# Kernel optimization log

Hardware: AMD Instinct MI355X
Metric: run time of the kernel (lower is better)

## Reference

```python
import jax, jax.numpy as jnp
import numpy as np
from jax import lax
from jax.scipy.special import logsumexp

N = 1024   # keypoints image 0
M = 1024   # keypoints image 1
D = 256    # descriptor dim
H = 4      # attention heads
L = 18     # GNN layers ('self','cross')*9
ITERS = 100
KENC = [4, 32, 64, 128, 256]


def conv1(x, w, b):
    # 1x1 Conv1d == channel matmul: x [b,c,n], w [o,c], b [o]
    return jnp.einsum('oc,bcn->bon', w, x) + b[None, :, None]


def inorm(x, eps=1e-5):
    # InstanceNorm1d (affine=False): normalize over length per (b, c)
    m = jnp.mean(x, axis=-1, keepdims=True)
    v = jnp.var(x, axis=-1, keepdims=True)
    return (x - m) * lax.rsqrt(v + eps)


def attention_block(x, src, pw, pb, mw, mb):
    b, d, _ = x.shape
    dh = d // H
    q = conv1(x, pw[0], pb[0]).reshape(b, dh, H, -1)
    k = conv1(src, pw[1], pb[1]).reshape(b, dh, H, -1)
    v = conv1(src, pw[2], pb[2]).reshape(b, dh, H, -1)
    s = jnp.einsum('bdhn,bdhm->bhnm', q, k) / (dh ** 0.5)
    p = jax.nn.softmax(s, axis=-1)
    o = jnp.einsum('bhnm,bdhm->bdhn', p, v).reshape(b, d, -1)
    return conv1(o, mw, mb)


def prop(x, src, i, Pw, Pb, Mw, Mb, W0, B0, W1, B1):
    msg = attention_block(x, src, Pw[i], Pb[i], Mw[i], Mb[i])
    h = jnp.concatenate([x, msg], axis=1)          # [b, 2D, n]
    h = jax.nn.relu(inorm(conv1(h, W0[i], B0[i])))
    return conv1(h, W1[i], B1[i])


def sinkhorn(Z, log_mu, log_nu, iters):
    def step(carry, _):
        u, v = carry
        u = log_mu - logsumexp(Z + v[:, None, :], axis=2)
        v = log_nu - logsumexp(Z + u[:, :, None], axis=1)
        return (u, v), None
    init = (jnp.zeros_like(log_mu), jnp.zeros_like(log_nu))
    (u, v), _ = lax.scan(jax.checkpoint(step), init, None, length=iters)
    return Z + u[:, :, None] + v[:, None, :]


def log_optimal_transport(scores, alpha, iters):
    b, m, n = scores.shape
    bins0 = jnp.broadcast_to(alpha, (b, m, 1))
    bins1 = jnp.broadcast_to(alpha, (b, 1, n))
    binsA = jnp.broadcast_to(alpha, (b, 1, 1))
    couplings = jnp.concatenate([
        jnp.concatenate([scores, bins0], axis=-1),
        jnp.concatenate([bins1, binsA], axis=-1)], axis=1)  # [b, m+1, n+1]
    norm = np.float32(-np.log(m + n))
    log_mu = jnp.concatenate([jnp.full((m,), norm, scores.dtype),
                              jnp.array([np.log(n)], scores.dtype) + norm])
    log_nu = jnp.concatenate([jnp.full((n,), norm, scores.dtype),
                              jnp.array([np.log(m)], scores.dtype) + norm])
    log_mu = jnp.broadcast_to(log_mu[None], (b, m + 1))
    log_nu = jnp.broadcast_to(log_nu[None], (b, n + 1))
    Z = sinkhorn(couplings, log_mu, log_nu, iters)
    return Z - norm


def setup_inputs() -> dict:
    key = jax.random.key(0)
    ks = iter(jax.random.split(key, 64))
    w = lambda shape, s=0.02: jax.random.normal(next(ks), shape, jnp.float32) * s
    inp = {
        'keypoints0': jax.random.normal(next(ks), (1, N, 3), jnp.float32),
        'keypoints1': jax.random.normal(next(ks), (1, M, 3), jnp.float32),
        'descriptors0': jax.random.normal(next(ks), (1, D, N), jnp.float32),
        'descriptors1': jax.random.normal(next(ks), (1, D, M), jnp.float32),
        'scores0': jax.random.uniform(next(ks), (1, N), jnp.float32),
        'scores1': jax.random.uniform(next(ks), (1, M), jnp.float32),
    }
    for i in range(4):
        inp[f'kenc_w{i}'] = w((KENC[i + 1], KENC[i]), 0.1)
        inp[f'kenc_b{i}'] = jnp.zeros((KENC[i + 1],), jnp.float32)
    inp['gnn_proj_w'] = w((L, 3, D, D))
    inp['gnn_proj_b'] = jnp.zeros((L, 3, D), jnp.float32)
    inp['gnn_merge_w'] = w((L, D, D))
    inp['gnn_merge_b'] = jnp.zeros((L, D), jnp.float32)
    inp['gnn_mlp_w0'] = w((L, 2 * D, 2 * D))
    inp['gnn_mlp_b0'] = jnp.zeros((L, 2 * D), jnp.float32)
    inp['gnn_mlp_w1'] = w((L, D, 2 * D))
    inp['gnn_mlp_b1'] = jnp.zeros((L, D), jnp.float32)
    inp['final_w'] = w((D, D))
    inp['final_b'] = jnp.zeros((D,), jnp.float32)
    inp['bin_score'] = jnp.float32(1.0)
    return inp


def reference(keypoints0, keypoints1, descriptors0, descriptors1, scores0, scores1,
              kenc_w0, kenc_b0, kenc_w1, kenc_b1, kenc_w2, kenc_b2, kenc_w3, kenc_b3,
              gnn_proj_w, gnn_proj_b, gnn_merge_w, gnn_merge_b,
              gnn_mlp_w0, gnn_mlp_b0, gnn_mlp_w1, gnn_mlp_b1,
              final_w, final_b, bin_score):
    def kenc(kpts, sc):
        h = jnp.concatenate([jnp.swapaxes(kpts, 1, 2), sc[:, None, :]], axis=1)  # [b,4,n]
        h = jax.nn.relu(inorm(conv1(h, kenc_w0, kenc_b0)))
        h = jax.nn.relu(inorm(conv1(h, kenc_w1, kenc_b1)))
        h = jax.nn.relu(inorm(conv1(h, kenc_w2, kenc_b2)))
        return conv1(h, kenc_w3, kenc_b3)

    d0 = descriptors0 + kenc(keypoints0, scores0)
    d1 = descriptors1 + kenc(keypoints1, scores1)
    for i in range(L):  # even: self, odd: cross
        cross = (i % 2 == 1)
        s0 = d1 if cross else d0
        s1 = d0 if cross else d1
        delta0 = prop(d0, s0, i, gnn_proj_w, gnn_proj_b, gnn_merge_w, gnn_merge_b,
                      gnn_mlp_w0, gnn_mlp_b0, gnn_mlp_w1, gnn_mlp_b1)
        delta1 = prop(d1, s1, i, gnn_proj_w, gnn_proj_b, gnn_merge_w, gnn_merge_b,
                      gnn_mlp_w0, gnn_mlp_b0, gnn_mlp_w1, gnn_mlp_b1)
        d0, d1 = d0 + delta0, d1 + delta1
    md0 = conv1(d0, final_w, final_b)
    md1 = conv1(d1, final_w, final_b)
    scores = jnp.einsum('bdn,bdm->bnm', md0, md1) / (D ** 0.5)
    return log_optimal_transport(scores, bin_score, ITERS)
```

## Files before the change

kernel.cpp:

```cpp
#include <hip/hip_runtime.h>
#include <cstddef>

#define TPB 256

typedef _Float16 f16;
typedef _Float16 f16x4 __attribute__((ext_vector_type(4)));
typedef _Float16 f16x8 __attribute__((ext_vector_type(8)));
typedef float f32x4 __attribute__((ext_vector_type(4)));
typedef unsigned long long u64;

__device__ __forceinline__ float block_sum(float v, float* red) {
  int tid = threadIdx.x;
  red[tid] = v; __syncthreads();
#pragma unroll
  for (int off = 128; off > 0; off >>= 1) {
    if (tid < off) red[tid] += red[tid + off];
    __syncthreads();
  }
  float r = red[0];
  __syncthreads();
  return r;
}

__global__ __launch_bounds__(TPB) void build_h0(const float* __restrict__ kp0,
                                                const float* __restrict__ kp1,
                                                const float* __restrict__ sc0,
                                                const float* __restrict__ sc1,
                                                float* __restrict__ h0) {
  int n = blockIdx.x * TPB + threadIdx.x;
  int im = blockIdx.y;
  const float* kp = im ? kp1 : kp0;
  const float* sc = im ? sc1 : sc0;
  float* h = h0 + (size_t)im * 4096;
  h[n]        = kp[n * 3 + 0];
  h[1024 + n] = kp[n * 3 + 1];
  h[2048 + n] = kp[n * 3 + 2];
  h[3072 + n] = sc[n];
}

template<bool NORMRELU, bool RESID>
__global__ __launch_bounds__(TPB) void chanconv(const float* __restrict__ W,
                                                const float* __restrict__ bias,
                                                const float* __restrict__ in, long instride,
                                                const float* res0, const float* res1,
                                                float* __restrict__ out, long outstride, int C) {
  int o = blockIdx.x, im = blockIdx.y, tid = threadIdx.x;
  const float* inp = in + (long)im * instride;
  __shared__ float Ws[128];
  __shared__ float red[TPB];
  for (int c = tid; c < C; c += TPB) Ws[c] = W[(long)o * C + c];
  __syncthreads();
  float b = bias[o];
  float4 acc = {b, b, b, b};
  for (int c = 0; c < C; ++c) {
    float w = Ws[c];
    float4 v = *(const float4*)(inp + (long)c * 1024 + tid * 4);
    acc.x += w * v.x; acc.y += w * v.y; acc.z += w * v.z; acc.w += w * v.w;
  }
  float* orow = out + (long)im * outstride + (long)o * 1024;
  if (NORMRELU) {
    float s = acc.x + acc.y + acc.z + acc.w;
    float mean = block_sum(s, red) * (1.f / 1024.f);
    float dx = acc.x - mean, dy = acc.y - mean, dz = acc.z - mean, dw = acc.w - mean;
    float var = block_sum(dx * dx + dy * dy + dz * dz + dw * dw, red) * (1.f / 1024.f);
    float rstd = rsqrtf(var + 1e-5f);
    float4 o4 = {fmaxf(dx * rstd, 0.f), fmaxf(dy * rstd, 0.f),
                 fmaxf(dz * rstd, 0.f), fmaxf(dw * rstd, 0.f)};
    *(float4*)(orow + tid * 4) = o4;
  } else {
    if (RESID) {
      const float* res = im ? res1 : res0;
      float4 r = *(const float4*)(res + (long)o * 1024 + tid * 4);
      acc.x += r.x; acc.y += r.y; acc.z += r.z; acc.w += r.w;
    }
    *(float4*)(orow + tid * 4) = acc;
  }
}

struct GBH {
  const void* A; const void* B; const void* B2; void* C;
  const float* bias; const float* res; const float* mu; const float* rs;
  void* o2a; void* o2b; int coff; int pad;
};
struct GBN { GBH g[18]; };

#define F_BNORM   1
#define F_BCONCAT 2
#define F_BADD    4
#define F_CD16    8
#define F_RES     16
#define F_OUT2    32
#define F_CSCAT   64
#define F_BNORM2  128
#define F_ACONCAT 256
#define F_BMIX    512
#define F_STATS   1024

template<int BM, int BN, int ASRC, int BSRC, int FLAGS>
__global__ __launch_bounds__(TPB) void gemmh(GBN gbs, int K, int lda, int ldb,
                                             int ldc, float alpha, int ksplit) {
  constexpr int WM = BM / 32;
  constexpr int NWN = 4 / WM;
  constexpr int WN = BN / NWN;
  constexpr int NFR = WN / 16;
  GBH g = gbs.g[blockIdx.z];
  const int tid = threadIdx.x;
  const int lane = tid & 63, wid = tid >> 6;
  const int wm = wid / NWN, wn = wid % NWN;
  const int m0 = blockIdx.y * BM, n0 = blockIdx.x * BN;
  __shared__ f16 As[BM][36];
  __shared__ f16 Bs[BN][36];
  f32x4 acc[2][NFR];
#pragma unroll
  for (int i = 0; i < 2; ++i)
#pragma unroll
    for (int j = 0; j < NFR; ++j) acc[i][j] = (f32x4){0.f, 0.f, 0.f, 0.f};

  for (int k0 = 0; k0 < K; k0 += 32) {
    if constexpr (ASRC == 0) {
      if constexpr (BM == 64) {
        const int m = tid >> 2, k4 = (tid & 3) * 8;
        const float* ap;
        if constexpr ((FLAGS & F_ACONCAT) != 0) {
          if (k0 >= ksplit)
            ap = (const float*)g.o2a + (long)(m0 + m) * 256 + (k0 - ksplit) + k4;
          else
            ap = (const float*)g.A + (long)(m0 + m) * lda + k0 + k4;
        } else {
          ap = (const float*)g.A + (long)(m0 + m) * lda + k0 + k4;
        }
        float4 u0 = *(const float4*)ap, u1 = *(const float4*)(ap + 4);
        f16x4 h0 = {(f16)u0.x, (f16)u0.y, (f16)u0.z, (f16)u0.w};
        f16x4 h1 = {(f16)u1.x, (f16)u1.y, (f16)u1.z, (f16)u1.w};
        *(f16x4*)&As[m][k4] = h0;
        *(f16x4*)&As[m][k4 + 4] = h1;
      } else {
        const int m = tid >> 3, k4 = (tid & 7) * 4;
        const float* ap = (const float*)g.A + (long)(m0 + m) * lda + k0 + k4;
        float4 u0 = *(const float4*)ap;
        f16x4 h0 = {(f16)u0.x, (f16)u0.y, (f16)u0.z, (f16)u0.w};
        *(f16x4*)&As[m][k4] = h0;
      }
    } else if constexpr (ASRC == 1) {
      const int k = tid >> 3, mg = (tid & 7) * 8;
      const f16* ap = (const f16*)g.A + (long)(k0 + k) * lda + m0 + mg;
      f16x8 h = *(const f16x8*)ap;
#pragma unroll
      for (int j = 0; j < 8; ++j) As[mg + j][k] = h[j];
    } else {
      const int m = tid >> 2, k4 = (tid & 3) * 8;
      const f16* ap = (const f16*)g.A + (long)(m0 + m) * lda + k0 + k4;
      f16x8 h = *(const f16x8*)ap;
      const float M = g.mu[m0 + m], Iv = g.rs[m0 + m];
      f16x4 h0, h1;
#pragma unroll
      for (int j = 0; j < 4; ++j) h0[j] = (f16)(__expf((float)h[j] - M) * Iv);
#pragma unroll
      for (int j = 0; j < 4; ++j) h1[j] = (f16)(__expf((float)h[j + 4] - M) * Iv);
      *(f16x4*)&As[m][k4] = h0;
      *(f16x4*)&As[m][k4 + 4] = h1;
    }
#pragma unroll
    for (int r = 0; r < BN / 64; ++r) {
      if constexpr (BSRC == 0) {
        bool f16path = false;
        if constexpr ((FLAGS & F_BMIX) != 0) f16path = (k0 >= ksplit);
        if (f16path) {
          const int n = (tid >> 2) + r * 64, k4b = (tid & 3) * 8;
          const long off = (long)(n0 + n) * 256 + (k0 - ksplit) + k4b;
          f16x8 h = *(const f16x8*)((const f16*)g.B2 + off)
                  + *(const f16x8*)((const f16*)g.o2b + off);
          f16x4 h0 = {h[0], h[1], h[2], h[3]};
          f16x4 h1 = {h[4], h[5], h[6], h[7]};
          *(f16x4*)&Bs[n][k4b] = h0;
          *(f16x4*)&Bs[n][k4b + 4] = h1;
        } else {
          const int k = tid >> 3, ng = (tid & 7) * 8 + r * 64;
          const int kg = k0 + k;
          const float* bp;
          if constexpr ((FLAGS & F_BCONCAT) != 0)
            bp = (kg < ksplit) ? ((const float*)g.B + (long)kg * ldb)
                               : ((const float*)g.B2 + (long)(kg - ksplit) * ldb);
          else
            bp = (const float*)g.B + (long)kg * ldb;
          float4 u0 = *(const float4*)(bp + n0 + ng);
          float4 u1 = *(const float4*)(bp + n0 + ng + 4);
          Bs[ng + 0][k] = (f16)u0.x; Bs[ng + 1][k] = (f16)u0.y;
          Bs[ng + 2][k] = (f16)u0.z; Bs[ng + 3][k] = (f16)u0.w;
          Bs[ng + 4][k] = (f16)u1.x; Bs[ng + 5][k] = (f16)u1.y;
          Bs[ng + 6][k] = (f16)u1.z; Bs[ng + 7][k] = (f16)u1.w;
        }
      } else if constexpr (BSRC == 1) {
        const int k = tid >> 3, ng = (tid & 7) * 8 + r * 64;
        const int kg = k0 + k;
        f16x8 h = *(const f16x8*)((const f16*)g.B + (long)kg * ldb + n0 + ng);
        if constexpr ((FLAGS & (F_BNORM | F_BNORM2)) != 0) {
          float mean, rstd;
          if constexpr ((FLAGS & F_BNORM2) != 0) {
            float s1 = g.mu[kg], s2 = g.rs[kg];
            mean = s1 * (1.f / 1024.f);
            rstd = rsqrtf(fmaxf(s2 * (1.f / 1024.f) - mean * mean, 0.f) + 1e-5f);
          } else {
            mean = g.mu[kg]; rstd = g.rs[kg];
          }
#pragma unroll
          for (int j = 0; j < 8; ++j)
            h[j] = (f16)fmaxf(((float)h[j] - mean) * rstd, 0.f);
        }
#pragma unroll
        for (int j = 0; j < 8; ++j) Bs[ng + j][k] = h[j];
      } else {
        const int n = (tid >> 2) + r * 64, k4 = (tid & 3) * 8;
        const f16* bp = (const f16*)g.B + (long)(n0 + n) * ldb + k0 + k4;
        f16x8 h = *(const f16x8*)bp;
        if constexpr ((FLAGS & F_BADD) != 0) {
          f16x8 h2 = *(const f16x8*)((const f16*)g.B2 + (long)(n0 + n) * ldb + k0 + k4);
          h = h + h2;
        }
        f16x4 h0 = {h[0], h[1], h[2], h[3]};
        f16x4 h1 = {h[4], h[5], h[6], h[7]};
        *(f16x4*)&Bs[n][k4] = h0;
        *(f16x4*)&Bs[n][k4 + 4] = h1;
      }
    }
    __syncthreads();
#pragma unroll
    for (int ks = 0; ks < 2; ++ks) {
      const int kof = ks * 16 + ((lane >> 4) << 2);
      f16x4 a[2], b[NFR];
      a[0] = *(const f16x4*)&As[wm * 32 + (lane & 15)][kof];
      a[1] = *(const f16x4*)&As[wm * 32 + 16 + (lane & 15)][kof];
#pragma unroll
      for (int fn = 0; fn < NFR; ++fn)
        b[fn] = *(const f16x4*)&Bs[wn * WN + fn * 16 + (lane & 15)][kof];
#pragma unroll
      for (int fm = 0; fm < 2; ++fm)
#pragma unroll
        for (int fn = 0; fn < NFR; ++fn)
          acc[fm][fn] = __builtin_amdgcn_mfma_f32_16x16x16f16(a[fm], b[fn], acc[fm][fn], 0, 0, 0);
    }
    __syncthreads();
  }

  const int r0 = (lane >> 4) << 2, cn = lane & 15;
#pragma unroll
  for (int fm = 0; fm < 2; ++fm) {
#pragma unroll
    for (int r = 0; r < 4; ++r) {
      const int m = m0 + wm * 32 + fm * 16 + r0 + r;
      const float bi = g.bias ? g.bias[m] : 0.f;
      float s1 = 0.f, s2 = 0.f;
#pragma unroll
      for (int fn = 0; fn < NFR; ++fn) {
        const int n = n0 + wn * WN + fn * 16 + cn;
        float v = acc[fm][fn][r] * alpha + bi;
        if constexpr ((FLAGS & F_RES) != 0) v += g.res[(long)m * ldc + n];
        if constexpr ((FLAGS & F_OUT2) != 0) {
          ((float*)g.C)[(long)m * 1028 + n] = v;
          ((f16*)g.o2a)[(long)m * 1028 + n] = (f16)v;
          ((f16*)g.o2b)[(long)n * 1028 + m] = (f16)v;
        } else if constexpr ((FLAGS & F_CSCAT) != 0) {
          ((f16*)g.C)[(long)m * ldc + g.coff + 4 * n] = (f16)v;
        } else if constexpr ((FLAGS & F_CD16) != 0) {
          ((f16*)g.C)[(long)m * ldc + n] = (f16)v;
        } else {
          ((float*)g.C)[(long)m * ldc + n] = v;
        }
        if constexpr ((FLAGS & F_STATS) != 0) { s1 += v; s2 += v * v; }
      }
      if constexpr ((FLAGS & F_STATS) != 0) {
#pragma unroll
        for (int off = 1; off < 16; off <<= 1) {
          s1 += __shfl_xor(s1, off);
          s2 += __shfl_xor(s2, off);
        }
        if ((lane & 15) == 0) {
          atomicAdd((float*)g.mu + m, s1);
          atomicAdd((float*)g.rs + m, s2);
        }
      }
    }
  }
}

__global__ __launch_bounds__(TPB) void rowlse_h(const f16* __restrict__ S,
                                                float* __restrict__ Mrow,
                                                float* __restrict__ Inv) {
  int row = blockIdx.x * 4 + (threadIdx.x >> 6);
  int lane = threadIdx.x & 63;
  const f16x8* p = (const f16x8*)(S + (long)row * 1024);
  f16x8 v0 = p[lane], v1 = p[lane + 64];
  float m = -1e30f;
#pragma unroll
  for (int j = 0; j < 8; ++j)
    m = fmaxf(m, fmaxf((float)v0[j], (float)v1[j]));
#pragma unroll
  for (int off = 32; off > 0; off >>= 1) m = fmaxf(m, __shfl_xor(m, off));
  float s = 0.f;
#pragma unroll
  for (int j = 0; j < 8; ++j)
    s += __expf((float)v0[j] - m) + __expf((float)v1[j] - m);
#pragma unroll
  for (int off = 32; off > 0; off >>= 1) s += __shfl_xor(s, off);
  if (lane == 0) { Mrow[row] = m; Inv[row] = 1.f / s; }
}

__global__ __launch_bounds__(TPB) void zero_buf(float* __restrict__ p, int n) {
  int i = blockIdx.x * TPB + threadIdx.x;
  if (i < n) p[i] = 0.f;
}

__global__ __launch_bounds__(TPB) void bf_prep(const float* __restrict__ mlp_w0,
                                               const float* __restrict__ mlp_b0,
                                               const float* __restrict__ merge_b,
                                               float* __restrict__ bfB) {
  int idx = blockIdx.x * TPB + threadIdx.x;
  int l = idx >> 9, m = idx & 511;
  const float* wrow = mlp_w0 + (size_t)l * 262144 + (size_t)m * 512 + 256;
  const float* mb = merge_b + (size_t)l * 256;
  float s = mlp_b0[(size_t)l * 512 + m];
  for (int j = 0; j < 256; ++j) s += wrow[j] * mb[j];
  bfB[idx] = s;
}

#define NORMC  (-7.62461899f)
#define LOGN   (6.93147181f)
#define LOG_MN (7.62461899f)
#define ZLD    1028
#define SINKB  64

__device__ __forceinline__ u64 llc_load64(const u64* p) {
  return __hip_atomic_load(p, __ATOMIC_RELAXED, __HIP_MEMORY_SCOPE_AGENT);
}
__device__ __forceinline__ void slot_store(u64* p, float v, unsigned gen) {
  union { float f; unsigned u; } c; c.f = v;
  u64 x = ((u64)gen << 32) | (u64)c.u;
  __hip_atomic_store(p, x, __ATOMIC_RELAXED, __HIP_MEMORY_SCOPE_AGENT);
}
__device__ __forceinline__ float slot_val(u64 x) {
  union { unsigned u; float f; } c; c.u = (unsigned)x;
  return c.f;
}

__global__ __launch_bounds__(TPB) void fill_bins(float* __restrict__ Z,
                                                 const float* __restrict__ alpha_p,
                                                 u64* __restrict__ uS,
                                                 u64* __restrict__ vS) {
  float a = *alpha_p;
  int t = blockIdx.x * TPB + threadIdx.x;
  if (t <= 1024) {
    Z[(long)t * ZLD + 1024] = a;
    Z[(long)1024 * ZLD + t] = a;
    slot_store(uS + t, 0.f, 0u);
    slot_store(vS + t, 0.f, 0u);
  }
}

__device__ __forceinline__ void sink_half(const f16x8 zreg[4][2],
                                          const u64* __restrict__ w,
                                          u64* __restrict__ out,
                                          unsigned rgen, int tid, int gw, int lane,
                                          float alpha, float* __restrict__ lds) {
  __syncthreads();
#pragma unroll
  for (int q = 0; q < 4; ++q) {
    const int s = tid + q * TPB;
    u64 x;
    do { x = llc_load64(w + s); } while ((unsigned)(x >> 32) != rgen);
    lds[s] = slot_val(x);
  }
  if (tid == 0) {
    u64 x;
    do { x = llc_load64(w + 1024); } while ((unsigned)(x >> 32) != rgen);
    lds[1024] = slot_val(x);
  }
  __syncthreads();

  float vv[16];
#pragma unroll
  for (int t = 0; t < 16; ++t) vv[t] = lds[lane + 64 * t];
  const float w1024 = lds[1024];
  const float binv = alpha + w1024;
  const unsigned wgen = rgen + 1;

  float res[4];
#pragma unroll
  for (int r = 0; r < 4; ++r) {
    float val[16];
    float m = binv;
#pragma unroll
    for (int t = 0; t < 16; ++t) {
      val[t] = (float)zreg[r][t >> 3][t & 7] + vv[t];
      m = fmaxf(m, val[t]);
    }
#pragma unroll
    for (int off = 32; off > 0; off >>= 1) m = fmaxf(m, __shfl_xor(m, off));
    float s = 0.f;
#pragma unroll
    for (int t = 0; t < 16; ++t) s += __expf(val[t] - m);
#pragma unroll
    for (int off = 32; off > 0; off >>= 1) s += __shfl_xor(s, off);
    s += __expf(binv - m);
    res[r] = NORMC - (m + logf(s));
  }
  float myv = (lane == 0) ? res[0] : (lane == 1) ? res[1]
            : (lane == 2) ? res[2] : res[3];
  if (lane < 4) slot_store(out + 4 * gw + lane, myv, wgen);

  if (gw == 0) {
    float m = w1024;
#pragma unroll
    for (int t = 0; t < 16; ++t) m = fmaxf(m, vv[t]);
#pragma unroll
    for (int off = 32; off > 0; off >>= 1) m = fmaxf(m, __shfl_xor(m, off));
    float s = 0.f;
#pragma unroll
    for (int t = 0; t < 16; ++t) s += __expf(vv[t] - m);
#pragma unroll
    for (int off = 32; off > 0; off >>= 1) s += __shfl_xor(s, off);
    s += __expf(w1024 - m);
    if (lane == 0)
      slot_store(out + 1024, NORMC + LOGN - (alpha + m + logf(s)), wgen);
  }
}

__global__ __launch_bounds__(TPB) void sink_persist(const f16* __restrict__ Zh,
                                                    const f16* __restrict__ Zth,
                                                    u64* __restrict__ uS,
                                                    u64* __restrict__ vS,
                                                    const float* __restrict__ alpha_p) {
  __shared__ float lds[ZLD];
  const int tid = threadIdx.x;
  const int lane = tid & 63;
  const int gw = blockIdx.x * 4 + (tid >> 6);
  const float alpha = *alpha_p;

  f16x8 zr[4][2], zt[4][2];
#pragma unroll
  for (int r = 0; r < 4; ++r) {
    const long row = 4 * gw + r;
    const f16* zp = Zh + row * ZLD;
    const f16* ztp = Zth + row * ZLD;
#pragma unroll
    for (int hh = 0; hh < 2; ++hh)
#pragma unroll
      for (int j = 0; j < 8; ++j) {
        zr[r][hh][j] = zp[lane + 64 * (8 * hh + j)];
        zt[r][hh][j] = ztp[lane + 64 * (8 * hh + j)];
      }
  }

  unsigned gen = 0;
#pragma unroll 1
  for (int it = 0; it < 100; ++it) {
    sink_half(zr, vS, uS, gen, tid, gw, lane, alpha, lds);  ++gen;
    sink_half(zt, uS, vS, gen, tid, gw, lane, alpha, lds);  ++gen;
  }
}

__global__ __launch_bounds__(TPB) void assemble(const float* __restrict__ Z,
                                                const u64* __restrict__ uS,
                                                const u64* __restrict__ vS,
                                                float* __restrict__ out) {
  int idx = blockIdx.x * TPB + threadIdx.x;
  if (idx < 1025 * 1025) {
    int i = idx / 1025;
    int j = idx - i * 1025;
    out[idx] = Z[(long)i * ZLD + j] + slot_val(uS[i]) + slot_val(vS[j]) + LOG_MN;
  }
}

static inline GBH mkgb(const void* A, const void* B, void* C,
                       const float* bias = nullptr, const void* B2 = nullptr,
                       const float* res = nullptr,
                       const float* mu = nullptr, const float* rs = nullptr,
                       int coff = 0, void* o2a = nullptr, void* o2b = nullptr) {
  GBH g; g.A = A; g.B = B; g.B2 = B2; g.C = C; g.bias = bias; g.res = res;
  g.mu = mu; g.rs = rs; g.o2a = o2a; g.o2b = o2b; g.coff = coff; g.pad = 0;
  return g;
}

extern "C" void kernel_launch(void* const* d_in, const int* in_sizes, int n_in,
                              void* d_out, int out_size, void* d_ws, size_t ws_size,
                              hipStream_t stream) {
  const float* kp0     = (const float*)d_in[0];
  const float* kp1     = (const float*)d_in[1];
  const float* desc0   = (const float*)d_in[2];
  const float* desc1   = (const float*)d_in[3];
  const float* sc0     = (const float*)d_in[4];
  const float* sc1     = (const float*)d_in[5];
  const float* kw[4]   = {(const float*)d_in[6], (const float*)d_in[8],
                          (const float*)d_in[10], (const float*)d_in[12]};
  const float* kb[4]   = {(const float*)d_in[7], (const float*)d_in[9],
                          (const float*)d_in[11], (const float*)d_in[13]};
  const float* proj_w  = (const float*)d_in[14];
  const float* proj_b  = (const float*)d_in[15];
  const float* merge_w = (const float*)d_in[16];
  const float* merge_b = (const float*)d_in[17];
  const float* mlp_w0  = (const float*)d_in[18];
  const float* mlp_b0  = (const float*)d_in[19];
  const float* mlp_w1  = (const float*)d_in[20];
  const float* mlp_b1  = (const float*)d_in[21];
  const float* final_w = (const float*)d_in[22];
  const float* final_b = (const float*)d_in[23];
  const float* alpha_p = (const float*)d_in[24];

  float* p = (float*)d_ws;
  float* dA  = p; p += 524288;
  float* dB  = p; p += 524288;
  float* h0  = p; p += 8192;
  float* hb1 = p; p += 262144;
  float* hb2 = p; p += 131072;
  float* Mrw = p; p += 8192;
  float* Inv = p; p += 8192;
  float* Zb  = p; p += 1053700;
  float* WfB = p; p += 2359296;
  float* bfB = p; p += 9216;
  float* SS1 = p; p += 18432;
  float* SS2 = p; p += 18432;
  u64* uS = (u64*)p; p += 2056;
  u64* vS = (u64*)p; p += 2056;
  f16* qkvh = (f16*)p; p += 786432;
  f16* Sh   = (f16*)p; p += 4194304;
  f16* oAh  = (f16*)p; p += 262144;
  f16* oBh  = (f16*)p; p += 262144;
  f16* tbh  = (f16*)p; p += 524288;
  f16* mdbh = (f16*)p; p += 262144;
  f16* Zh   = (f16*)p; p += 526852;
  f16* Zth  = (f16*)p; p += 526852;
  size_t need_bytes = (size_t)(p - (float*)d_ws) * sizeof(float);
  if (ws_size < need_bytes) return;

  const long DSTR = 262144;

  zero_buf<<<144, TPB, 0, stream>>>(SS1, 36864);
  {
    GBN gb{};
    for (int l = 0; l < 18; ++l)
      gb.g[l] = mkgb(mlp_w0 + (size_t)l * 262144 + 256, merge_w + (size_t)l * 65536,
                     WfB + (size_t)l * 131072);
    gemmh<64, 64, 0, 0, 0><<<dim3(4, 8, 18), TPB, 0, stream>>>(
        gb, 256, 512, 256, 256, 1.f, 0);
  }
  bf_prep<<<36, TPB, 0, stream>>>(mlp_w0, mlp_b0, merge_b, bfB);

  build_h0<<<dim3(4, 2), TPB, 0, stream>>>(kp0, kp1, sc0, sc1, h0);
  chanconv<true, false><<<dim3(32, 2),  TPB, 0, stream>>>(kw[0], kb[0], h0,  4096,   nullptr, nullptr, hb1, 32768,  4);
  chanconv<true, false><<<dim3(64, 2),  TPB, 0, stream>>>(kw[1], kb[1], hb1, 32768,  nullptr, nullptr, hb2, 65536,  32);
  chanconv<true, false><<<dim3(128, 2), TPB, 0, stream>>>(kw[2], kb[2], hb2, 65536,  nullptr, nullptr, hb1, 131072, 64);
  chanconv<false, true><<<dim3(256, 2), TPB, 0, stream>>>(kw[3], kb[3], hb1, 131072, desc0,   desc1,   dA,  DSTR,   128);

  float* dc = dA;
  float* dn = dB;
  for (int i = 0; i < 18; ++i) {
    bool cross = (i & 1) != 0;
    const float* xs[2] = {dc, dc + DSTR};
    const float* ss2[2] = {cross ? xs[1] : xs[0], cross ? xs[0] : xs[1]};

    {
      GBN gb{};
      for (int im = 0; im < 2; ++im)
        for (int pp = 0; pp < 3; ++pp)
          gb.g[im * 3 + pp] = mkgb(proj_w + (size_t)(i * 3 + pp) * 65536,
                                   (pp == 0 ? xs[im] : ss2[im]),
                                   qkvh + (size_t)(im * 3 + pp) * DSTR,
                                   proj_b + (size_t)(i * 3 + pp) * 256);
      gemmh<32, 128, 0, 0, F_CD16><<<dim3(8, 8, 6), TPB, 0, stream>>>(
          gb, 256, 256, 1024, 1024, 1.f, 0);
    }
    {
      GBN gb{};
      for (int im = 0; im < 2; ++im)
        for (int h = 0; h < 4; ++h)
          gb.g[im * 4 + h] = mkgb(qkvh + (size_t)(im * 3 + 0) * DSTR + h * 1024,
                                  qkvh + (size_t)(im * 3 + 1) * DSTR + h * 1024,
                                  Sh + (size_t)(im * 4 + h) * 1048576);
      gemmh<64, 128, 1, 1, F_CD16><<<dim3(8, 16, 8), TPB, 0, stream>>>(
          gb, 64, 4096, 4096, 1024, 0.125f, 0);
    }
    rowlse_h<<<2048, TPB, 0, stream>>>(Sh, Mrw, Inv);
    {
      GBN gb{};
      for (int kh = 0; kh < 2; ++kh)
        for (int imh = 0; imh < 8; ++imh) {
          int im = imh >> 2, h = imh & 3;
          gb.g[kh * 8 + imh] = mkgb(Sh + (size_t)imh * 1048576 + kh * 512,
                                    qkvh + (size_t)(im * 3 + 2) * DSTR + h * 1024 + kh * 512,
                                    (kh ? oBh : oAh) + (size_t)im * 262144,
                                    nullptr, nullptr, nullptr,
                                    Mrw + imh * 1024, Inv + imh * 1024, h);
        }
      gemmh<64, 64, 2, 2, F_CD16 | F_CSCAT><<<dim3(1, 16, 16), TPB, 0, stream>>>(
          gb, 512, 1024, 4096, 256, 1.f, 0);
    }
    {
      GBN gb{};
      for (int im = 0; im < 2; ++im)
        gb.g[im] = mkgb(mlp_w0 + (size_t)i * 262144, xs[im],
                        tbh + (size_t)im * 524288, bfB + (size_t)i * 512,
                        oAh + (size_t)im * 262144, nullptr,
                        SS1 + (size_t)i * 1024 + im * 512,
                        SS2 + (size_t)i * 1024 + im * 512,
                        0, WfB + (size_t)i * 131072, oBh + (size_t)im * 262144);
      gemmh<64, 64, 0, 0, F_CD16 | F_ACONCAT | F_BMIX | F_STATS>
          <<<dim3(16, 8, 2), TPB, 0, stream>>>(
          gb, 512, 512, 1024, 1024, 1.f, 256);
    }
    {
      GBN gb{};
      for (int im = 0; im < 2; ++im)
        gb.g[im] = mkgb(mlp_w1 + (size_t)i * 131072, tbh + (size_t)im * 524288,
                        dn + (size_t)im * DSTR, mlp_b1 + (size_t)i * 256,
                        nullptr, xs[im],
                        SS1 + (size_t)i * 1024 + im * 512,
                        SS2 + (size_t)i * 1024 + im * 512);
      gemmh<32, 64, 0, 1, F_BNORM2 | F_RES><<<dim3(16, 8, 2), TPB, 0, stream>>>(
          gb, 512, 512, 1024, 1024, 1.f, 0);
    }
    float* tmp = dc; dc = dn; dn = tmp;
  }

  {
    GBN gb{};
    for (int im = 0; im < 2; ++im)
      gb.g[im] = mkgb(final_w, dc + (size_t)im * DSTR, mdbh + (size_t)im * 262144,
                      final_b);
    gemmh<32, 64, 0, 0, F_CD16><<<dim3(16, 8, 2), TPB, 0, stream>>>(
        gb, 256, 256, 1024, 1024, 1.f, 0);
  }
  {
    GBN gb{};
    gb.g[0] = mkgb(mdbh, mdbh + 262144, Zb, nullptr, nullptr, nullptr,
                   nullptr, nullptr, 0, Zh, Zth);
    gemmh<64, 64, 1, 1, F_OUT2><<<dim3(16, 16, 1), TPB, 0, stream>>>(
        gb, 256, 1024, 1024, ZLD, 0.0625f, 0);
  }
  fill_bins<<<5, TPB, 0, stream>>>(Zb, alpha_p, uS, vS);

  sink_persist<<<SINKB, TPB, 0, stream>>>(Zh, Zth, uS, vS, alpha_p);

  assemble<<<4105, TPB, 0, stream>>>(Zb, uS, vS, (float*)d_out);
}
```

Measured before the change: 2.264 ms.

## Batch Sinkhorn polling loads, double-buffer LDS, and shrink PV GEMM tile rows

The persistent Sinkhorn kernel now issues all four slot loads together per polling round instead of spinning on each slot in turn. It also ping-pongs between two LDS buffers, which lets it drop the leading __syncthreads in each half-iteration. Separately, the softmax-fused PV GEMM switches to a BM=32 tile, with a new A-load path and twice as many row blocks, to put more blocks on the GPU. The LDS double-buffering relies on the alternating halves never overlapping in their buffer use.

```diff
diff --git a/kernel.cpp b/kernel.cpp
--- a/kernel.cpp
+++ b/kernel.cpp
@@ -148,17 +148,28 @@
 #pragma unroll
       for (int j = 0; j < 8; ++j) As[mg + j][k] = h[j];
     } else {
-      const int m = tid >> 2, k4 = (tid & 3) * 8;
-      const f16* ap = (const f16*)g.A + (long)(m0 + m) * lda + k0 + k4;
-      f16x8 h = *(const f16x8*)ap;
-      const float M = g.mu[m0 + m], Iv = g.rs[m0 + m];
-      f16x4 h0, h1;
-#pragma unroll
-      for (int j = 0; j < 4; ++j) h0[j] = (f16)(__expf((float)h[j] - M) * Iv);
-#pragma unroll
-      for (int j = 0; j < 4; ++j) h1[j] = (f16)(__expf((float)h[j + 4] - M) * Iv);
-      *(f16x4*)&As[m][k4] = h0;
-      *(f16x4*)&As[m][k4 + 4] = h1;
+      if constexpr (BM == 64) {
+        const int m = tid >> 2, k4 = (tid & 3) * 8;
+        const f16* ap = (const f16*)g.A + (long)(m0 + m) * lda + k0 + k4;
+        f16x8 h = *(const f16x8*)ap;
+        const float M = g.mu[m0 + m], Iv = g.rs[m0 + m];
+        f16x4 h0, h1;
+#pragma unroll
+        for (int j = 0; j < 4; ++j) h0[j] = (f16)(__expf((float)h[j] - M) * Iv);
+#pragma unroll
+        for (int j = 0; j < 4; ++j) h1[j] = (f16)(__expf((float)h[j + 4] - M) * Iv);
+        *(f16x4*)&As[m][k4] = h0;
+        *(f16x4*)&As[m][k4 + 4] = h1;
+      } else {
+        const int m = tid >> 3, k4 = (tid & 7) * 4;
+        const f16* ap = (const f16*)g.A + (long)(m0 + m) * lda + k0 + k4;
+        f16x4 h = *(const f16x4*)ap;
+        const float M = g.mu[m0 + m], Iv = g.rs[m0 + m];
+        f16x4 h0;
+#pragma unroll
+        for (int j = 0; j < 4; ++j) h0[j] = (f16)(__expf((float)h[j] - M) * Iv);
+        *(f16x4*)&As[m][k4] = h0;
+      }
     }
 #pragma unroll
     for (int r = 0; r < BN / 64; ++r) {
@@ -361,19 +372,25 @@
                                           u64* __restrict__ out,
                                           unsigned rgen, int tid, int gw, int lane,
                                           float alpha, float* __restrict__ lds) {
-  __syncthreads();
-#pragma unroll
-  for (int q = 0; q < 4; ++q) {
-    const int s = tid + q * TPB;
-    u64 x;
-    do { x = llc_load64(w + s); } while ((unsigned)(x >> 32) != rgen);
-    lds[s] = slot_val(x);
-  }
-  if (tid == 0) {
-    u64 x;
-    do { x = llc_load64(w + 1024); } while ((unsigned)(x >> 32) != rgen);
-    lds[1024] = slot_val(x);
-  }
+  u64 x0, x1, x2, x3, xb = 0;
+  bool ok = false;
+  while (!ok) {
+    x0 = llc_load64(w + tid);
+    x1 = llc_load64(w + tid + 256);
+    x2 = llc_load64(w + tid + 512);
+    x3 = llc_load64(w + tid + 768);
+    ok = ((unsigned)(x0 >> 32) == rgen) & ((unsigned)(x1 >> 32) == rgen)
+       & ((unsigned)(x2 >> 32) == rgen) & ((unsigned)(x3 >> 32) == rgen);
+    if (tid == 0) {
+      xb = llc_load64(w + 1024);
+      ok = ok & ((unsigned)(xb >> 32) == rgen);
+    }
+  }
+  lds[tid]       = slot_val(x0);
+  lds[tid + 256] = slot_val(x1);
+  lds[tid + 512] = slot_val(x2);
+  lds[tid + 768] = slot_val(x3);
+  if (tid == 0) lds[1024] = slot_val(xb);
   __syncthreads();
 
   float vv[16];
@@ -429,7 +446,8 @@
                                                     u64* __restrict__ uS,
                                                     u64* __restrict__ vS,
                                                     const float* __restrict__ alpha_p) {
-  __shared__ float lds[ZLD];
+  __shared__ float lds0[ZLD];
+  __shared__ float lds1[ZLD];
   const int tid = threadIdx.x;
   const int lane = tid & 63;
   const int gw = blockIdx.x * 4 + (tid >> 6);
@@ -453,8 +471,8 @@
   unsigned gen = 0;
 #pragma unroll 1
   for (int it = 0; it < 100; ++it) {
-    sink_half(zr, vS, uS, gen, tid, gw, lane, alpha, lds);  ++gen;
-    sink_half(zt, uS, vS, gen, tid, gw, lane, alpha, lds);  ++gen;
+    sink_half(zr, vS, uS, gen, tid, gw, lane, alpha, lds0);  ++gen;
+    sink_half(zt, uS, vS, gen, tid, gw, lane, alpha, lds1);  ++gen;
   }
 }
 
@@ -590,7 +608,7 @@
                                     nullptr, nullptr, nullptr,
                                     Mrw + imh * 1024, Inv + imh * 1024, h);
         }
-      gemmh<64, 64, 2, 2, F_CD16 | F_CSCAT><<<dim3(1, 16, 16), TPB, 0, stream>>>(
+      gemmh<32, 64, 2, 2, F_CD16 | F_CSCAT><<<dim3(1, 32, 16), TPB, 0, stream>>>(
           gb, 512, 1024, 4096, 256, 1.f, 0);
     }
     {
```

Result: faster. 2.134 ms (-5.8%).
